# Optimization experiments

Measured on AMD Instinct MI355X. Metric: run time of the kernel, lower is better.

## Reference

```python
import jax, jax.numpy as jnp
import numpy as np

WEIGHT_STD = 0.1
WEIGHT_STD2 = 2.0 * WEIGHT_STD ** 2  # 0.02
CONF_THRESH = 0.9


def setup_inputs() -> dict:
    key = jax.random.key(0)
    k0, k1, k2, k3 = jax.random.split(key, 4)
    B, N, V, J = 1, 32768, 10475, 55
    # skinning weights: nonnegative, rows sum to 1 (as in SMPL-X)
    lbs_weights = jax.random.uniform(k0, (V, J), dtype=jnp.float32)
    lbs_weights = lbs_weights / jnp.sum(lbs_weights, -1, keepdims=True)
    verts_transform = jax.random.normal(k1, (B, V, 4, 4), dtype=jnp.float32)
    points = jax.random.normal(k2, (B, N, 3), dtype=jnp.float32)
    template_points = jax.random.normal(k3, (B, V, 3), dtype=jnp.float32)
    return {
        "lbs_weights": lbs_weights,
        "verts_transform": verts_transform,
        "points": points,
        "template_points": template_points,
        "K": 6,
    }


def _knn(points, template_points, K):
    """Brute-force KNN; squared L2 dists like pytorch3d knn_points. -> dists, idx [B,N,K] ascending."""
    p2 = jnp.sum(points * points, -1)[:, :, None]            # [B,N,1]
    t2 = jnp.sum(template_points * template_points, -1)[:, None, :]  # [B,1,V]
    cross = jnp.einsum("bnd,bvd->bnv", points, template_points)     # [B,N,V]
    d2 = jnp.maximum(p2 + t2 - 2.0 * cross, 0.0)
    neg_d, idx = jax.lax.top_k(-d2, K)  # largest of -d2 == smallest d2, sorted ascending
    return -neg_d, idx


def reference(lbs_weights, verts_transform, points, template_points, K):
    B = points.shape[0]
    neighbs_dist, neighbs = _knn(points, template_points, K)  # [B,N,K]

    # gather skinning weights of the K neighbors: [B,N,K,J]
    w_n = lbs_weights[neighbs]
    # confidence: neighbors whose lbs weights agree with the nearest one
    conf = jnp.exp(-jnp.sum(jnp.abs(w_n - w_n[..., 0:1, :]), -1) / WEIGHT_STD2)
    conf = (conf > CONF_THRESH).astype(neighbs_dist.dtype)
    w = jnp.exp(-neighbs_dist) * conf
    w = w / jnp.sum(w, -1, keepdims=True)  # [B,N,K]; k=0 conf always 1 -> sum > 0

    # gather per-vertex 4x4 transforms: [B,N,K,4,4]
    vt_n = verts_transform[jnp.arange(B)[:, None, None], neighbs]
    xyz_transform = jnp.sum(w[..., None, None] * vt_n, axis=2)   # [B,N,4,4]
    xyz_dist = jnp.sum(w * neighbs_dist, axis=2, keepdims=True)  # [B,N,1]
    return xyz_dist, xyz_transform
```

## Files before the change

kernel.cpp:

```cpp
#include <hip/hip_runtime.h>
#include <math.h>

#pragma clang fp contract(off)

#define NPTS  32768
#define NV    10475
#define JW    55
#define TILE  1024
#define TIT   16
#define NT    11
#define BLOCK 256
#define R     8
#define PPB   32
#define CAP   22
#define FINF  3.4e38f
#define GMARG 0.00025f

#define FOR8(M) M(0) M(1) M(2) M(3) M(4) M(5) M(6) M(7)

#define LTL(dd, vv, D, I) ((dd) < (D) || ((dd) == (D) && (vv) < (I)))
#define INSL6(dd, vv, D0,I0,D1,I1,D2,I2,D3,I3,D4,I4,D5,I5) \
  if (LTL(dd, vv, D5, I5)) { \
    if (LTL(dd, vv, D4, I4)) { D5=D4; I5=I4; \
      if (LTL(dd, vv, D3, I3)) { D4=D3; I4=I3; \
        if (LTL(dd, vv, D2, I2)) { D3=D2; I3=I2; \
          if (LTL(dd, vv, D1, I1)) { D2=D1; I2=I1; \
            if (LTL(dd, vv, D0, I0)) { D1=D0; I1=I0; D0=(dd); I0=(vv); } \
            else { D1=(dd); I1=(vv); } \
          } else { D2=(dd); I2=(vv); } \
        } else { D3=(dd); I3=(vv); } \
      } else { D4=(dd); I4=(vv); } \
    } else { D5=(dd); I5=(vv); } \
  }

__global__ __launch_bounds__(BLOCK, 4)
void scarf_knn_lbs(const float* __restrict__ lbs,
                   const float* __restrict__ vtf,
                   const float* __restrict__ pts,
                   const float* __restrict__ tpl,
                   float* __restrict__ out_dist,
                   float* __restrict__ out_tf)
{
    __shared__ float4 s_tile[2][TILE];
    __shared__ float  s_bd[PPB][CAP];
    __shared__ int    s_bi[PPB][CAP];
    __shared__ int    s_cnt[PPB];
    __shared__ float  s_td[PPB][6];
    __shared__ int    s_ti[PPB][6];

    const int tid = threadIdx.x;
    const int h   = tid & 63;
    const int w   = tid >> 6;
    const int lp  = w * R;
    const int p0  = blockIdx.x * PPB + lp;

    if (tid < PPB) s_cnt[tid] = 0;

    #define DECLP(r) \
      const float Px##r = 2.0f * pts[(p0+(r))*3+0]; \
      const float Py##r = 2.0f * pts[(p0+(r))*3+1]; \
      const float Pz##r = 2.0f * pts[(p0+(r))*3+2]; \
      const float q##r  = (Px##r*Px##r + Py##r*Py##r) + Pz##r*Pz##r;
    FOR8(DECLP)

    float gx[4], gy[4], gz[4];

    #define STAGE_ISSUE(t_) { \
      _Pragma("unroll") \
      for (int k = 0; k < 4; ++k) { \
        const int j = (t_) * TILE + k * BLOCK + tid; \
        if (j < NV) { gx[k] = tpl[j*3+0]; gy[k] = tpl[j*3+1]; gz[k] = tpl[j*3+2]; } \
        else        { gx[k] = 1.0e6f;    gy[k] = 1.0e6f;    gz[k] = 1.0e6f;    } } }

    #define STAGE_WRITE(dst_) { \
      _Pragma("unroll") \
      for (int k = 0; k < 4; ++k) { \
        const float X = gx[k]+gx[k], Y = gy[k]+gy[k], Z = gz[k]+gz[k]; \
        s_tile[dst_][k * BLOCK + tid] = make_float4(X, Y, Z, (X*X + Y*Y) + Z*Z); } }

    #define DECLM(r) float m##r = FINF;
    FOR8(DECLM)

    #define EVP1(r) { \
      const float Ca = fmaf(Pz##r, ta.z, fmaf(Py##r, ta.y, Px##r * ta.x)); \
      const float da = fmaf(-2.0f, Ca, ta.w); \
      const float Cb = fmaf(Pz##r, tb.z, fmaf(Py##r, tb.y, Px##r * tb.x)); \
      const float db = fmaf(-2.0f, Cb, tb.w); \
      m##r = fminf(fminf(m##r, da), db); }

    STAGE_ISSUE(0); STAGE_WRITE(0); __syncthreads();
    for (int t = 0; t < NT; ++t) {
        if (t + 1 < NT) STAGE_ISSUE(t + 1);
        const float4* bp = s_tile[t & 1];
        #pragma unroll 2
        for (int it = 0; it < TIT; it += 2) {
            const float4 ta = bp[it * 64 + h];
            const float4 tb = bp[(it + 1) * 64 + h];
            FOR8(EVP1)
        }
        if (t + 1 < NT) { STAGE_WRITE((t + 1) & 1); __syncthreads(); }
    }

    #define DECLT(r) float G##r; { \
      float v = m##r; float M; \
      _Pragma("unroll") \
      for (int rep = 0; rep < 6; ++rep) { \
        M = v; \
        M = fminf(M, __shfl_xor(M, 1)); \
        M = fminf(M, __shfl_xor(M, 2)); \
        M = fminf(M, __shfl_xor(M, 4)); \
        M = fminf(M, __shfl_xor(M, 8)); \
        M = fminf(M, __shfl_xor(M, 16)); \
        M = fminf(M, __shfl_xor(M, 32)); \
        if (rep < 5) v = (v == M) ? FINF : v; \
      } \
      G##r = M + GMARG; }
    FOR8(DECLT)

    __syncthreads();

    #define EVP2(r) { \
      const float C  = fmaf(Pz##r, tv.z, fmaf(Py##r, tv.y, Px##r * tv.x)); \
      const float dp = fmaf(-2.0f, C, tv.w); \
      if (dp <= G##r) { \
        const float de = fmaf(-2.0f, C, q##r + tv.w);   \
        const int k = atomicAdd(&s_cnt[lp+(r)], 1); \
        if (k < CAP) { s_bd[lp+(r)][k] = fmaxf(de, 0.0f); s_bi[lp+(r)][k] = tb + it*64 + h; } } }

    STAGE_ISSUE(0); STAGE_WRITE(0); __syncthreads();
    for (int t = 0; t < NT; ++t) {
        if (t + 1 < NT) STAGE_ISSUE(t + 1);
        const float4* bp = s_tile[t & 1];
        const int tb = t * TILE;
        #pragma unroll 4
        for (int it = 0; it < TIT; ++it) {
            const float4 tv = bp[it * 64 + h];
            FOR8(EVP2)
        }
        if (t + 1 < NT) { STAGE_WRITE((t + 1) & 1); __syncthreads(); }
    }

    if (h < 8) {
        const int lpr = lp + h;
        float D0=FINF,D1=FINF,D2=FINF,D3=FINF,D4=FINF,D5=FINF;
        int   I0=-1,I1=-1,I2=-1,I3=-1,I4=-1,I5=-1;
        const int cc = s_cnt[lpr];
        const int c  = (cc < CAP) ? cc : CAP;
        for (int k = 0; k < c; ++k) {
            const float dd = s_bd[lpr][k]; const int vv = s_bi[lpr][k];
            INSL6(dd, vv, D0,I0,D1,I1,D2,I2,D3,I3,D4,I4,D5,I5);
        }
        s_td[lpr][0]=D0; s_td[lpr][1]=D1; s_td[lpr][2]=D2;
        s_td[lpr][3]=D3; s_td[lpr][4]=D4; s_td[lpr][5]=D5;
        s_ti[lpr][0]=I0; s_ti[lpr][1]=I1; s_ti[lpr][2]=I2;
        s_ti[lpr][3]=I3; s_ti[lpr][4]=I4; s_ti[lpr][5]=I5;
    }

    {
        const int r  = h >> 3;
        const int l  = h & 7;
        const int lpr = lp + r;
        const int i0 = s_ti[lpr][0];
        const int i1 = s_ti[lpr][1], i2 = s_ti[lpr][2], i3 = s_ti[lpr][3];
        const int i4 = s_ti[lpr][4], i5 = s_ti[lpr][5];
        float s1 = 0.0f, s2 = 0.0f, s3 = 0.0f, s4 = 0.0f, s5 = 0.0f;
        for (int j = l; j < JW; j += 8) {
            const float w0 = lbs[(long)i0 * JW + j];
            s1 += fabsf(lbs[(long)i1 * JW + j] - w0);
            s2 += fabsf(lbs[(long)i2 * JW + j] - w0);
            s3 += fabsf(lbs[(long)i3 * JW + j] - w0);
            s4 += fabsf(lbs[(long)i4 * JW + j] - w0);
            s5 += fabsf(lbs[(long)i5 * JW + j] - w0);
        }
        s1 += __shfl_xor(s1,1); s1 += __shfl_xor(s1,2); s1 += __shfl_xor(s1,4);
        s2 += __shfl_xor(s2,1); s2 += __shfl_xor(s2,2); s2 += __shfl_xor(s2,4);
        s3 += __shfl_xor(s3,1); s3 += __shfl_xor(s3,2); s3 += __shfl_xor(s3,4);
        s4 += __shfl_xor(s4,1); s4 += __shfl_xor(s4,2); s4 += __shfl_xor(s4,4);
        s5 += __shfl_xor(s5,1); s5 += __shfl_xor(s5,2); s5 += __shfl_xor(s5,4);
        const float sv = (l==0)?s1:(l==1)?s2:(l==2)?s3:(l==3)?s4:s5;
        const bool pred = (l < 5) && (expf(-sv / 0.02f) > 0.9f);
        const unsigned long long bal = __ballot(pred);

        #pragma unroll
        for (int t = 0; t < 2; ++t) {
            const int re  = (h >> 4) + 4 * t;
            const int e   = h & 15;
            const int lpe = lp + re;
            const int P   = p0 + re;
            const unsigned mr = (unsigned)(bal >> (re * 8)) & 31u;

            const float d0 = 0.25f * s_td[lpe][0], d1 = 0.25f * s_td[lpe][1];
            const float d2 = 0.25f * s_td[lpe][2], d3 = 0.25f * s_td[lpe][3];
            const float d4 = 0.25f * s_td[lpe][4], d5 = 0.25f * s_td[lpe][5];
            const int   j0 = s_ti[lpe][0], j1 = s_ti[lpe][1], j2 = s_ti[lpe][2];
            const int   j3 = s_ti[lpe][3], j4 = s_ti[lpe][4], j5 = s_ti[lpe][5];

            const float w0 = expf(-d0);
            const float w1 = (mr & 1u)  ? expf(-d1) : 0.0f;
            const float w2 = (mr & 2u)  ? expf(-d2) : 0.0f;
            const float w3 = (mr & 4u)  ? expf(-d3) : 0.0f;
            const float w4 = (mr & 8u)  ? expf(-d4) : 0.0f;
            const float w5 = (mr & 16u) ? expf(-d5) : 0.0f;
            const float inv = 1.0f / (w0 + w1 + w2 + w3 + w4 + w5);
            const float n0 = w0*inv, n1 = w1*inv, n2 = w2*inv;
            const float n3 = w3*inv, n4 = w4*inv, n5 = w5*inv;

            if (e == 0)
                out_dist[P] = n0*d0 + n1*d1 + n2*d2 + n3*d3 + n4*d4 + n5*d5;

            float acc = n0 * vtf[j0*16 + e];
            acc = fmaf(n1, vtf[j1*16 + e], acc);
            acc = fmaf(n2, vtf[j2*16 + e], acc);
            acc = fmaf(n3, vtf[j3*16 + e], acc);
            acc = fmaf(n4, vtf[j4*16 + e], acc);
            acc = fmaf(n5, vtf[j5*16 + e], acc);
            out_tf[P*16 + e] = acc;
        }
    }
}

extern "C" void kernel_launch(void* const* d_in, const int* in_sizes, int n_in,
                              void* d_out, int out_size, void* d_ws, size_t ws_size,
                              hipStream_t stream) {
    const float* lbs = (const float*)d_in[0];
    const float* vtf = (const float*)d_in[1];
    const float* pts = (const float*)d_in[2];
    const float* tpl = (const float*)d_in[3];
    float* out = (float*)d_out;
    scarf_knn_lbs<<<NPTS / PPB, BLOCK, 0, stream>>>(lbs, vtf, pts, tpl, out, out + NPTS);
}
```

Measured before the change: 122.4 us.

## Fuse two-pass KNN into single pass with progressively tightened candidate threshold

Replaces the full min-distance pass followed by a full candidate-collection pass with one pass over the templates. A provisional threshold is seeded from the first two tiles and re-tightened every few tiles from per-lane running minima. The tile size is halved and the candidate buffer grown to 64 slots to absorb the extra candidates a looser early threshold admits. This roughly halves the distance arithmetic and shared-memory traffic, in exchange for more shared atomics early on and a risk of overflowing the candidate buffer.

```diff
diff --git a/kernel.cpp b/kernel.cpp
--- a/kernel.cpp
+++ b/kernel.cpp
@@ -6,13 +6,12 @@
 #define NPTS  32768
 #define NV    10475
 #define JW    55
-#define TILE  1024
-#define TIT   16
-#define NT    11
+#define TILE  512
+#define NT    21
 #define BLOCK 256
 #define R     8
 #define PPB   32
-#define CAP   22
+#define CAP   64
 #define FINF  3.4e38f
 #define GMARG 0.00025f
 
@@ -63,45 +62,45 @@
       const float q##r  = (Px##r*Px##r + Py##r*Py##r) + Pz##r*Pz##r;
     FOR8(DECLP)
 
-    float gx[4], gy[4], gz[4];
-
+    float gx[2], gy[2], gz[2];
     #define STAGE_ISSUE(t_) { \
       _Pragma("unroll") \
-      for (int k = 0; k < 4; ++k) { \
+      for (int k = 0; k < 2; ++k) { \
         const int j = (t_) * TILE + k * BLOCK + tid; \
         if (j < NV) { gx[k] = tpl[j*3+0]; gy[k] = tpl[j*3+1]; gz[k] = tpl[j*3+2]; } \
         else        { gx[k] = 1.0e6f;    gy[k] = 1.0e6f;    gz[k] = 1.0e6f;    } } }
-
     #define STAGE_WRITE(dst_) { \
       _Pragma("unroll") \
-      for (int k = 0; k < 4; ++k) { \
+      for (int k = 0; k < 2; ++k) { \
         const float X = gx[k]+gx[k], Y = gy[k]+gy[k], Z = gz[k]+gz[k]; \
         s_tile[dst_][k * BLOCK + tid] = make_float4(X, Y, Z, (X*X + Y*Y) + Z*Z); } }
 
     #define DECLM(r) float m##r = FINF;
     FOR8(DECLM)
 
-    #define EVP1(r) { \
+    #define EVI(r) { \
       const float Ca = fmaf(Pz##r, ta.z, fmaf(Py##r, ta.y, Px##r * ta.x)); \
       const float da = fmaf(-2.0f, Ca, ta.w); \
       const float Cb = fmaf(Pz##r, tb.z, fmaf(Py##r, tb.y, Px##r * tb.x)); \
       const float db = fmaf(-2.0f, Cb, tb.w); \
       m##r = fminf(fminf(m##r, da), db); }
 
-    STAGE_ISSUE(0); STAGE_WRITE(0); __syncthreads();
-    for (int t = 0; t < NT; ++t) {
-        if (t + 1 < NT) STAGE_ISSUE(t + 1);
-        const float4* bp = s_tile[t & 1];
-        #pragma unroll 2
-        for (int it = 0; it < TIT; it += 2) {
-            const float4 ta = bp[it * 64 + h];
-            const float4 tb = bp[(it + 1) * 64 + h];
-            FOR8(EVP1)
-        }
-        if (t + 1 < NT) { STAGE_WRITE((t + 1) & 1); __syncthreads(); }
-    }
-
-    #define DECLT(r) float G##r; { \
+    #define EVG(r) { \
+      const float Ca = fmaf(Pz##r, ta.z, fmaf(Py##r, ta.y, Px##r * ta.x)); \
+      const float da = fmaf(-2.0f, Ca, ta.w); \
+      if (da <= U##r) { \
+        const float de = fmaf(-2.0f, Ca, q##r + ta.w); \
+        const int k = atomicAdd(&s_cnt[lp+(r)], 1); \
+        if (k < CAP) { s_bd[lp+(r)][k] = fmaxf(de, 0.0f); s_bi[lp+(r)][k] = ia; } } \
+      const float Cb = fmaf(Pz##r, tb.z, fmaf(Py##r, tb.y, Px##r * tb.x)); \
+      const float db = fmaf(-2.0f, Cb, tb.w); \
+      if (db <= U##r) { \
+        const float de = fmaf(-2.0f, Cb, q##r + tb.w); \
+        const int k = atomicAdd(&s_cnt[lp+(r)], 1); \
+        if (k < CAP) { s_bd[lp+(r)][k] = fmaxf(de, 0.0f); s_bi[lp+(r)][k] = ib; } } \
+      m##r = fminf(fminf(m##r, da), db); }
+
+    #define UPDT(r) { \
       float v = m##r; float M; \
       _Pragma("unroll") \
       for (int rep = 0; rep < 6; ++rep) { \
@@ -114,30 +113,39 @@
         M = fminf(M, __shfl_xor(M, 32)); \
         if (rep < 5) v = (v == M) ? FINF : v; \
       } \
-      G##r = M + GMARG; }
-    FOR8(DECLT)
-
+      U##r = M + GMARG; }
+
+    STAGE_ISSUE(0); STAGE_WRITE(0);
+    STAGE_ISSUE(1); STAGE_WRITE(1);
     __syncthreads();
-
-    #define EVP2(r) { \
-      const float C  = fmaf(Pz##r, tv.z, fmaf(Py##r, tv.y, Px##r * tv.x)); \
-      const float dp = fmaf(-2.0f, C, tv.w); \
-      if (dp <= G##r) { \
-        const float de = fmaf(-2.0f, C, q##r + tv.w);   \
-        const int k = atomicAdd(&s_cnt[lp+(r)], 1); \
-        if (k < CAP) { s_bd[lp+(r)][k] = fmaxf(de, 0.0f); s_bi[lp+(r)][k] = tb + it*64 + h; } } }
-
-    STAGE_ISSUE(0); STAGE_WRITE(0); __syncthreads();
+    #pragma unroll
+    for (int b = 0; b < 2; ++b) {
+        const float4* bp = s_tile[b];
+        #pragma unroll
+        for (int itp = 0; itp < 4; ++itp) {
+            const float4 ta = bp[(2*itp    ) * 64 + h];
+            const float4 tb = bp[(2*itp + 1) * 64 + h];
+            FOR8(EVI)
+        }
+    }
+
+    #define DECLU(r) float U##r; UPDT(r);
+    FOR8(DECLU)
+
     for (int t = 0; t < NT; ++t) {
-        if (t + 1 < NT) STAGE_ISSUE(t + 1);
+        if (t >= 1 && t + 1 < NT) STAGE_ISSUE(t + 1);
         const float4* bp = s_tile[t & 1];
-        const int tb = t * TILE;
-        #pragma unroll 4
-        for (int it = 0; it < TIT; ++it) {
-            const float4 tv = bp[it * 64 + h];
-            FOR8(EVP2)
-        }
-        if (t + 1 < NT) { STAGE_WRITE((t + 1) & 1); __syncthreads(); }
+        #pragma unroll
+        for (int itp = 0; itp < 4; ++itp) {
+            const int ia = t * TILE + (2*itp) * 64 + h;
+            const int ib = ia + 64;
+            const float4 ta = bp[(2*itp    ) * 64 + h];
+            const float4 tb = bp[(2*itp + 1) * 64 + h];
+            FOR8(EVG)
+        }
+        if (t >= 1 && t + 1 < NT) STAGE_WRITE((t + 1) & 1);
+        __syncthreads();
+        if (t >= 4 && t % 3 == 1) { FOR8(UPDT) }
     }
 
     if (h < 8) {
```

Measured after the change: 253.4 us. 2.07x slower.

## Halve points per wave, fold -2 scaling into tile, retune epilogue lanes

Applied to the files above, without the earlier changes.

Cuts per-wave points from 8 to 4 and block points from 32 to 16. This doubles the grid, halves the tile size, and raises the launch-bounds occupancy target from 4 to 6. It pre-negates and doubles the template coordinates in shared memory, so the pass-one distance is a single chain of three FMAs with no separate -2 multiply. The epilogue is rebuilt around 16 lanes per point, one element of the transform per lane, and the gate margin is widened. The aim is fewer registers and higher occupancy, at the cost of loading each template tile twice as often per point and running more pass-two candidate insertions.

```diff
diff --git a/kernel.cpp b/kernel.cpp
--- a/kernel.cpp
+++ b/kernel.cpp
@@ -6,17 +6,16 @@
 #define NPTS  32768
 #define NV    10475
 #define JW    55
-#define TILE  1024
-#define TIT   16
-#define NT    11
+#define TILE  512
+#define NT    21
 #define BLOCK 256
-#define R     8
-#define PPB   32
+#define R     4
+#define PPB   16
 #define CAP   22
 #define FINF  3.4e38f
-#define GMARG 0.00025f
-
-#define FOR8(M) M(0) M(1) M(2) M(3) M(4) M(5) M(6) M(7)
+#define GMARG 0.001f
+
+#define FOR4(M) M(0) M(1) M(2) M(3)
 
 #define LTL(dd, vv, D, I) ((dd) < (D) || ((dd) == (D) && (vv) < (I)))
 #define INSL6(dd, vv, D0,I0,D1,I1,D2,I2,D3,I3,D4,I4,D5,I5) \
@@ -33,7 +32,7 @@
     } else { D5=(dd); I5=(vv); } \
   }
 
-__global__ __launch_bounds__(BLOCK, 4)
+__global__ __launch_bounds__(BLOCK, 6)
 void scarf_knn_lbs(const float* __restrict__ lbs,
                    const float* __restrict__ vtf,
                    const float* __restrict__ pts,
@@ -61,42 +60,39 @@
       const float Py##r = 2.0f * pts[(p0+(r))*3+1]; \
       const float Pz##r = 2.0f * pts[(p0+(r))*3+2]; \
       const float q##r  = (Px##r*Px##r + Py##r*Py##r) + Pz##r*Pz##r;
-    FOR8(DECLP)
-
-    float gx[4], gy[4], gz[4];
-
+    FOR4(DECLP)
+
+    float gx[2], gy[2], gz[2];
     #define STAGE_ISSUE(t_) { \
       _Pragma("unroll") \
-      for (int k = 0; k < 4; ++k) { \
+      for (int k = 0; k < 2; ++k) { \
         const int j = (t_) * TILE + k * BLOCK + tid; \
         if (j < NV) { gx[k] = tpl[j*3+0]; gy[k] = tpl[j*3+1]; gz[k] = tpl[j*3+2]; } \
         else        { gx[k] = 1.0e6f;    gy[k] = 1.0e6f;    gz[k] = 1.0e6f;    } } }
-
     #define STAGE_WRITE(dst_) { \
       _Pragma("unroll") \
-      for (int k = 0; k < 4; ++k) { \
+      for (int k = 0; k < 2; ++k) { \
         const float X = gx[k]+gx[k], Y = gy[k]+gy[k], Z = gz[k]+gz[k]; \
-        s_tile[dst_][k * BLOCK + tid] = make_float4(X, Y, Z, (X*X + Y*Y) + Z*Z); } }
+        s_tile[dst_][k * BLOCK + tid] = \
+          make_float4(-(X+X), -(Y+Y), -(Z+Z), (X*X + Y*Y) + Z*Z); } }
 
     #define DECLM(r) float m##r = FINF;
-    FOR8(DECLM)
+    FOR4(DECLM)
 
     #define EVP1(r) { \
-      const float Ca = fmaf(Pz##r, ta.z, fmaf(Py##r, ta.y, Px##r * ta.x)); \
-      const float da = fmaf(-2.0f, Ca, ta.w); \
-      const float Cb = fmaf(Pz##r, tb.z, fmaf(Py##r, tb.y, Px##r * tb.x)); \
-      const float db = fmaf(-2.0f, Cb, tb.w); \
+      const float da = fmaf(Pz##r, ta.z, fmaf(Py##r, ta.y, fmaf(Px##r, ta.x, ta.w))); \
+      const float db = fmaf(Pz##r, tb.z, fmaf(Py##r, tb.y, fmaf(Px##r, tb.x, tb.w))); \
       m##r = fminf(fminf(m##r, da), db); }
 
     STAGE_ISSUE(0); STAGE_WRITE(0); __syncthreads();
     for (int t = 0; t < NT; ++t) {
         if (t + 1 < NT) STAGE_ISSUE(t + 1);
         const float4* bp = s_tile[t & 1];
-        #pragma unroll 2
-        for (int it = 0; it < TIT; it += 2) {
-            const float4 ta = bp[it * 64 + h];
-            const float4 tb = bp[(it + 1) * 64 + h];
-            FOR8(EVP1)
+        #pragma unroll
+        for (int itp = 0; itp < 4; ++itp) {
+            const float4 ta = bp[(2*itp    ) * 64 + h];
+            const float4 tb = bp[(2*itp + 1) * 64 + h];
+            FOR4(EVP1)
         }
         if (t + 1 < NT) { STAGE_WRITE((t + 1) & 1); __syncthreads(); }
     }
@@ -115,14 +111,15 @@
         if (rep < 5) v = (v == M) ? FINF : v; \
       } \
       G##r = M + GMARG; }
-    FOR8(DECLT)
+    FOR4(DECLT)
 
     __syncthreads();
 
     #define EVP2(r) { \
-      const float C  = fmaf(Pz##r, tv.z, fmaf(Py##r, tv.y, Px##r * tv.x)); \
-      const float dp = fmaf(-2.0f, C, tv.w); \
+      const float dp = fmaf(Pz##r, tv.z, fmaf(Py##r, tv.y, fmaf(Px##r, tv.x, tv.w))); \
       if (dp <= G##r) { \
+        const float Xr = -0.5f * tv.x, Yr = -0.5f * tv.y, Zr = -0.5f * tv.z; \
+        const float C  = fmaf(Pz##r, Zr, fmaf(Py##r, Yr, Px##r * Xr)); \
         const float de = fmaf(-2.0f, C, q##r + tv.w);   \
         const int k = atomicAdd(&s_cnt[lp+(r)], 1); \
         if (k < CAP) { s_bd[lp+(r)][k] = fmaxf(de, 0.0f); s_bi[lp+(r)][k] = tb + it*64 + h; } } }
@@ -132,15 +129,15 @@
         if (t + 1 < NT) STAGE_ISSUE(t + 1);
         const float4* bp = s_tile[t & 1];
         const int tb = t * TILE;
-        #pragma unroll 4
-        for (int it = 0; it < TIT; ++it) {
+        #pragma unroll
+        for (int it = 0; it < 8; ++it) {
             const float4 tv = bp[it * 64 + h];
-            FOR8(EVP2)
+            FOR4(EVP2)
         }
         if (t + 1 < NT) { STAGE_WRITE((t + 1) & 1); __syncthreads(); }
     }
 
-    if (h < 8) {
+    if (h < R) {
         const int lpr = lp + h;
         float D0=FINF,D1=FINF,D2=FINF,D3=FINF,D4=FINF,D5=FINF;
         int   I0=-1,I1=-1,I2=-1,I3=-1,I4=-1,I5=-1;
@@ -156,15 +153,15 @@
         s_ti[lpr][3]=I3; s_ti[lpr][4]=I4; s_ti[lpr][5]=I5;
     }
 
+    const int r  = h >> 4;
+    const int l  = h & 15;
+    const int lpr = lp + r;
+    const int i0 = s_ti[lpr][0];
+    const int i1 = s_ti[lpr][1], i2 = s_ti[lpr][2], i3 = s_ti[lpr][3];
+    const int i4 = s_ti[lpr][4], i5 = s_ti[lpr][5];
     {
-        const int r  = h >> 3;
-        const int l  = h & 7;
-        const int lpr = lp + r;
-        const int i0 = s_ti[lpr][0];
-        const int i1 = s_ti[lpr][1], i2 = s_ti[lpr][2], i3 = s_ti[lpr][3];
-        const int i4 = s_ti[lpr][4], i5 = s_ti[lpr][5];
         float s1 = 0.0f, s2 = 0.0f, s3 = 0.0f, s4 = 0.0f, s5 = 0.0f;
-        for (int j = l; j < JW; j += 8) {
+        for (int j = l; j < JW; j += 16) {
             const float w0 = lbs[(long)i0 * JW + j];
             s1 += fabsf(lbs[(long)i1 * JW + j] - w0);
             s2 += fabsf(lbs[(long)i2 * JW + j] - w0);
@@ -172,50 +169,41 @@
             s4 += fabsf(lbs[(long)i4 * JW + j] - w0);
             s5 += fabsf(lbs[(long)i5 * JW + j] - w0);
         }
-        s1 += __shfl_xor(s1,1); s1 += __shfl_xor(s1,2); s1 += __shfl_xor(s1,4);
-        s2 += __shfl_xor(s2,1); s2 += __shfl_xor(s2,2); s2 += __shfl_xor(s2,4);
-        s3 += __shfl_xor(s3,1); s3 += __shfl_xor(s3,2); s3 += __shfl_xor(s3,4);
-        s4 += __shfl_xor(s4,1); s4 += __shfl_xor(s4,2); s4 += __shfl_xor(s4,4);
-        s5 += __shfl_xor(s5,1); s5 += __shfl_xor(s5,2); s5 += __shfl_xor(s5,4);
+        s1 += __shfl_xor(s1,1); s1 += __shfl_xor(s1,2); s1 += __shfl_xor(s1,4); s1 += __shfl_xor(s1,8);
+        s2 += __shfl_xor(s2,1); s2 += __shfl_xor(s2,2); s2 += __shfl_xor(s2,4); s2 += __shfl_xor(s2,8);
+        s3 += __shfl_xor(s3,1); s3 += __shfl_xor(s3,2); s3 += __shfl_xor(s3,4); s3 += __shfl_xor(s3,8);
+        s4 += __shfl_xor(s4,1); s4 += __shfl_xor(s4,2); s4 += __shfl_xor(s4,4); s4 += __shfl_xor(s4,8);
+        s5 += __shfl_xor(s5,1); s5 += __shfl_xor(s5,2); s5 += __shfl_xor(s5,4); s5 += __shfl_xor(s5,8);
         const float sv = (l==0)?s1:(l==1)?s2:(l==2)?s3:(l==3)?s4:s5;
         const bool pred = (l < 5) && (expf(-sv / 0.02f) > 0.9f);
         const unsigned long long bal = __ballot(pred);
-
-        #pragma unroll
-        for (int t = 0; t < 2; ++t) {
-            const int re  = (h >> 4) + 4 * t;
-            const int e   = h & 15;
-            const int lpe = lp + re;
-            const int P   = p0 + re;
-            const unsigned mr = (unsigned)(bal >> (re * 8)) & 31u;
-
-            const float d0 = 0.25f * s_td[lpe][0], d1 = 0.25f * s_td[lpe][1];
-            const float d2 = 0.25f * s_td[lpe][2], d3 = 0.25f * s_td[lpe][3];
-            const float d4 = 0.25f * s_td[lpe][4], d5 = 0.25f * s_td[lpe][5];
-            const int   j0 = s_ti[lpe][0], j1 = s_ti[lpe][1], j2 = s_ti[lpe][2];
-            const int   j3 = s_ti[lpe][3], j4 = s_ti[lpe][4], j5 = s_ti[lpe][5];
-
-            const float w0 = expf(-d0);
-            const float w1 = (mr & 1u)  ? expf(-d1) : 0.0f;
-            const float w2 = (mr & 2u)  ? expf(-d2) : 0.0f;
-            const float w3 = (mr & 4u)  ? expf(-d3) : 0.0f;
-            const float w4 = (mr & 8u)  ? expf(-d4) : 0.0f;
-            const float w5 = (mr & 16u) ? expf(-d5) : 0.0f;
-            const float inv = 1.0f / (w0 + w1 + w2 + w3 + w4 + w5);
-            const float n0 = w0*inv, n1 = w1*inv, n2 = w2*inv;
-            const float n3 = w3*inv, n4 = w4*inv, n5 = w5*inv;
-
-            if (e == 0)
-                out_dist[P] = n0*d0 + n1*d1 + n2*d2 + n3*d3 + n4*d4 + n5*d5;
-
-            float acc = n0 * vtf[j0*16 + e];
-            acc = fmaf(n1, vtf[j1*16 + e], acc);
-            acc = fmaf(n2, vtf[j2*16 + e], acc);
-            acc = fmaf(n3, vtf[j3*16 + e], acc);
-            acc = fmaf(n4, vtf[j4*16 + e], acc);
-            acc = fmaf(n5, vtf[j5*16 + e], acc);
-            out_tf[P*16 + e] = acc;
-        }
+        const unsigned mr = (unsigned)(bal >> (r * 16)) & 31u;
+
+        const int P = p0 + r;
+        const float d0 = 0.25f * s_td[lpr][0], d1 = 0.25f * s_td[lpr][1];
+        const float d2 = 0.25f * s_td[lpr][2], d3 = 0.25f * s_td[lpr][3];
+        const float d4 = 0.25f * s_td[lpr][4], d5 = 0.25f * s_td[lpr][5];
+
+        const float w0 = expf(-d0);
+        const float w1 = (mr & 1u)  ? expf(-d1) : 0.0f;
+        const float w2 = (mr & 2u)  ? expf(-d2) : 0.0f;
+        const float w3 = (mr & 4u)  ? expf(-d3) : 0.0f;
+        const float w4 = (mr & 8u)  ? expf(-d4) : 0.0f;
+        const float w5 = (mr & 16u) ? expf(-d5) : 0.0f;
+        const float inv = 1.0f / (w0 + w1 + w2 + w3 + w4 + w5);
+        const float n0 = w0*inv, n1 = w1*inv, n2 = w2*inv;
+        const float n3 = w3*inv, n4 = w4*inv, n5 = w5*inv;
+
+        if (l == 0)
+            out_dist[P] = n0*d0 + n1*d1 + n2*d2 + n3*d3 + n4*d4 + n5*d5;
+
+        float acc = n0 * vtf[i0*16 + l];
+        acc = fmaf(n1, vtf[i1*16 + l], acc);
+        acc = fmaf(n2, vtf[i2*16 + l], acc);
+        acc = fmaf(n3, vtf[i3*16 + l], acc);
+        acc = fmaf(n4, vtf[i4*16 + l], acc);
+        acc = fmaf(n5, vtf[i5*16 + l], acc);
+        out_tf[P*16 + l] = acc;
     }
 }
 
```

New measurement: 114.7 us. 6.3% less time.
